# Performance work log

Measured on AMD Instinct MI355X. Metric: run time of the kernel, lower is better.

Reference implementation:

```python
import jax, jax.numpy as jnp
import numpy as np

B = 128
D_MODEL = 1024
D_HEAD = 1024


def setup_inputs() -> dict:
    key = jax.random.key(0)
    ks = jax.random.split(key, 12)
    w = 0.02  # weight init scale
    return {
        "x_t": jax.random.normal(ks[0], (B, D_MODEL), dtype=jnp.float32),
        "C_prev": jax.random.normal(ks[1], (B, D_HEAD, D_HEAD), dtype=jnp.float32) * 0.05,
        "n_prev": jax.random.normal(ks[2], (B, D_HEAD), dtype=jnp.float32) * 0.05,
        "m_prev": jax.random.normal(ks[3], (B,), dtype=jnp.float32),
        "W_q": jax.random.normal(ks[4], (D_HEAD, D_MODEL), dtype=jnp.float32) * w,
        "W_k": jax.random.normal(ks[5], (D_HEAD, D_MODEL), dtype=jnp.float32) * w,
        "W_v": jax.random.normal(ks[6], (D_HEAD, D_MODEL), dtype=jnp.float32) * w,
        "w_i_w": jax.random.normal(ks[7], (D_MODEL,), dtype=jnp.float32) * w,
        "w_i_b": jnp.zeros((), dtype=jnp.float32),
        "w_f_w": jax.random.normal(ks[8], (D_MODEL,), dtype=jnp.float32) * w,
        "w_f_b": jnp.zeros((), dtype=jnp.float32),
        "W_o_w": jax.random.normal(ks[9], (D_HEAD, D_MODEL), dtype=jnp.float32) * w,
        "W_o_b": jnp.zeros((D_HEAD,), dtype=jnp.float32),
        "out_proj_w": jax.random.normal(ks[10], (D_MODEL, D_HEAD), dtype=jnp.float32) * w,
    }


def reference(x_t, C_prev, n_prev, m_prev, W_q, W_k, W_v,
              w_i_w, w_i_b, w_f_w, w_f_b, W_o_w, W_o_b, out_proj_w):
    d_head = W_q.shape[0]
    scale = 1.0 / jnp.sqrt(jnp.asarray(d_head, dtype=x_t.dtype))

    # projections (nn.Linear: y = x @ W.T)
    q_t = (x_t @ W_q.T) * scale            # (B, d)
    k_t = (x_t @ W_k.T) * scale            # (B, d)
    v_t = x_t @ W_v.T                      # (B, d)
    z_i = x_t @ w_i_w + w_i_b              # (B,)
    z_f = x_t @ w_f_w + w_f_b              # (B,)

    # stabilized exp gating
    m_t = jnp.maximum(z_f + m_prev, z_i)   # (B,)
    i_p = jnp.exp(z_i - m_t)               # (B,)
    f_p = jnp.exp(z_f + m_prev - m_t)      # (B,)

    # rank-1 outer-product write to matrix memory
    outer = v_t[:, :, None] * k_t[:, None, :]                 # (B, d, d)
    C_t = f_p[:, None, None] * C_prev + i_p[:, None, None] * outer
    n_t = f_p[:, None] * n_prev + i_p[:, None] * k_t

    # matvec read + normalization
    o_t = jax.nn.sigmoid(x_t @ W_o_w.T + W_o_b)               # (B, d)
    Cq = jnp.einsum('bij,bj->bi', C_t, q_t)                   # (B, d)
    denom = jnp.maximum(jnp.abs(jnp.sum(n_t * q_t, axis=-1, keepdims=True)), 1.0)
    h_head = o_t * Cq / denom
    h_t = h_head @ out_proj_w.T                               # (B, d_model)
    return (h_t, C_t, n_t, m_t)
```

## Files before the change

### kernel.cpp

```cpp
#include <hip/hip_runtime.h>
#include <hip/hip_bf16.h>
#include <math.h>

#define B_SZ   128
#define D_DIM  1024

typedef float f32x4 __attribute__((ext_vector_type(4)));

#define WS_Q   0
#define WS_K   (131072)
#define WS_V   (262144)
#define WS_O   (393216)
#define WS_H   (524288)
#define WS_IP  (655360)
#define WS_FP  (655488)
#define WS_DEN (655616)

#define OUT_H  0
#define OUT_C  (131072)
#define OUT_N  (134348800)
#define OUT_M  (134479872)

__global__ __launch_bounds__(256) void gemm_proj(
    const float* __restrict__ x,
    const float* __restrict__ Wq, const float* __restrict__ Wk,
    const float* __restrict__ Wv, const float* __restrict__ Wo,
    const float* __restrict__ Wob,
    float* __restrict__ oq, float* __restrict__ okk,
    float* __restrict__ ov, float* __restrict__ oo)
{
    __shared__ float Xs[32][64];
    __shared__ float Ws[32][32];

    const int tid = threadIdx.x;
    const int m0 = blockIdx.y * 64;
    const int ng = blockIdx.x * 32;
    const int matsel = ng >> 10;
    const int n0 = ng & 1023;
    const float* __restrict__ W =
        (matsel == 0) ? Wq : (matsel == 1) ? Wk : (matsel == 2) ? Wv : Wo;

    const int tx = tid & 7;
    const int ty = tid >> 3;

    float acc[2][4] = {{0.f,0.f,0.f,0.f},{0.f,0.f,0.f,0.f}};

    for (int kp = 0; kp < 1024; kp += 32) {
        #pragma unroll
        for (int l = 0; l < 2; ++l) {
            int f = tid + l * 256;
            int row = f >> 3, c = f & 7;
            float4 v4 = *(const float4*)&x[(m0 + row) * 1024 + kp + 4 * c];
            Xs[4*c+0][row] = v4.x; Xs[4*c+1][row] = v4.y;
            Xs[4*c+2][row] = v4.z; Xs[4*c+3][row] = v4.w;
        }
        {
            int row = tid >> 3, c = tid & 7;
            float4 v4 = *(const float4*)&W[(n0 + row) * 1024 + kp + 4 * c];
            Ws[4*c+0][row] = v4.x; Ws[4*c+1][row] = v4.y;
            Ws[4*c+2][row] = v4.z; Ws[4*c+3][row] = v4.w;
        }
        __syncthreads();
        #pragma unroll
        for (int k = 0; k < 32; ++k) {
            float2 xv = *(const float2*)&Xs[k][2 * ty];
            float4 wv = *(const float4*)&Ws[k][4 * tx];
            acc[0][0] += xv.x * wv.x; acc[0][1] += xv.x * wv.y;
            acc[0][2] += xv.x * wv.z; acc[0][3] += xv.x * wv.w;
            acc[1][0] += xv.y * wv.x; acc[1][1] += xv.y * wv.y;
            acc[1][2] += xv.y * wv.z; acc[1][3] += xv.y * wv.w;
        }
        __syncthreads();
    }

    #pragma unroll
    for (int r = 0; r < 2; ++r) {
        int b = m0 + 2 * ty + r;
        #pragma unroll
        for (int i2 = 0; i2 < 4; ++i2) {
            int j = n0 + 4 * tx + i2;
            float v = acc[r][i2];
            if (matsel == 0)      oq[b * 1024 + j] = v * 0.03125f;
            else if (matsel == 1) okk[b * 1024 + j] = v * 0.03125f;
            else if (matsel == 2) ov[b * 1024 + j] = v;
            else { v += Wob[j]; oo[b * 1024 + j] = 1.0f / (1.0f + expf(-v)); }
        }
    }
}

__global__ __launch_bounds__(256) void gates_kernel(
    const float* __restrict__ x, const float* __restrict__ n_prev,
    const float* __restrict__ m_prev,
    const float* __restrict__ w_i, const float* __restrict__ b_i,
    const float* __restrict__ w_f, const float* __restrict__ b_f,
    const float* __restrict__ ws_k, const float* __restrict__ ws_q,
    float* __restrict__ out_n, float* __restrict__ out_m,
    float* __restrict__ ws_ip, float* __restrict__ ws_fp,
    float* __restrict__ ws_den)
{
    const int b = blockIdx.x;
    const int t = threadIdx.x;
    const int lane = t & 63, wave = t >> 6;

    __shared__ float red[8];
    __shared__ float bc[2];

    float4 xv = ((const float4*)(x + b * 1024))[t];
    float4 wi = ((const float4*)w_i)[t];
    float4 wf = ((const float4*)w_f)[t];
    float si = xv.x*wi.x + xv.y*wi.y + xv.z*wi.z + xv.w*wi.w;
    float sf = xv.x*wf.x + xv.y*wf.y + xv.z*wf.z + xv.w*wf.w;
    #pragma unroll
    for (int off = 32; off >= 1; off >>= 1) {
        si += __shfl_down(si, off);
        sf += __shfl_down(sf, off);
    }
    if (lane == 0) { red[wave] = si; red[4 + wave] = sf; }
    __syncthreads();
    if (t == 0) {
        float zi = red[0] + red[1] + red[2] + red[3] + b_i[0];
        float zf = red[4] + red[5] + red[6] + red[7] + b_f[0];
        float mp = m_prev[b];
        float mt = fmaxf(zf + mp, zi);
        float ip = expf(zi - mt);
        float fp = expf(zf + mp - mt);
        out_m[b] = mt; ws_ip[b] = ip; ws_fp[b] = fp;
        bc[0] = ip; bc[1] = fp;
    }
    __syncthreads();
    float ip = bc[0], fp = bc[1];
    float4 np = ((const float4*)(n_prev + b * 1024))[t];
    float4 kk = ((const float4*)(ws_k + b * 1024))[t];
    float4 qq = ((const float4*)(ws_q + b * 1024))[t];
    float4 nt;
    nt.x = fp * np.x + ip * kk.x;
    nt.y = fp * np.y + ip * kk.y;
    nt.z = fp * np.z + ip * kk.z;
    nt.w = fp * np.w + ip * kk.w;
    ((float4*)(out_n + b * 1024))[t] = nt;
    float sd = nt.x*qq.x + nt.y*qq.y + nt.z*qq.z + nt.w*qq.w;
    #pragma unroll
    for (int off = 32; off >= 1; off >>= 1) sd += __shfl_down(sd, off);
    if (lane == 0) red[wave] = sd;
    __syncthreads();
    if (t == 0) {
        float d = red[0] + red[1] + red[2] + red[3];
        ws_den[b] = fmaxf(fabsf(d), 1.0f);
    }
}

__global__ __launch_bounds__(256) void cell_kernel(
    const float* __restrict__ C_prev,
    const float* __restrict__ ws_k, const float* __restrict__ ws_q,
    const float* __restrict__ ws_v, const float* __restrict__ ws_o,
    const float* __restrict__ ws_ip, const float* __restrict__ ws_fp,
    const float* __restrict__ ws_den,
    float* __restrict__ out_C, float* __restrict__ ws_h)
{
    const int t    = threadIdx.x;
    const int lane = t & 63;
    const int wave = t >> 6;
    const int wglob = blockIdx.x * 4 + wave;
    const int r0 = wglob * 16;
    const int b  = r0 >> 10;

    const float fp   = ws_fp[b];
    const float ip   = ws_ip[b];
    const float rden = 1.0f / ws_den[b];

    const f32x4* qv = (const f32x4*)(ws_q + b * 1024);
    const f32x4* kv = (const f32x4*)(ws_k + b * 1024);
    f32x4 q4[4], k4[4];
    #pragma unroll
    for (int j = 0; j < 4; ++j) {
        q4[j] = qv[lane + 64 * j];
        k4[j] = kv[lane + 64 * j];
    }

    const f32x4* Cp = (const f32x4*)(C_prev + (size_t)r0 * 1024);
    f32x4*       Ct = (f32x4*)(out_C + (size_t)r0 * 1024);

    #define CELL_ROW(RR, CBUF)                                                \
    {                                                                         \
        const int row = r0 + (RR);                                            \
        const float coef = ip * ws_v[row];                                    \
        float s = 0.f;                                                        \
        _Pragma("unroll")                                                     \
        for (int j = 0; j < 4; ++j) {                                         \
            f32x4 r = fp * CBUF[j] + coef * k4[j];                            \
            __builtin_nontemporal_store(r, &Ct[(RR) * 256 + lane + 64 * j]);  \
            f32x4 d = r * q4[j];                                              \
            s += d.x + d.y + d.z + d.w;                                       \
        }                                                                     \
        _Pragma("unroll")                                                     \
        for (int off = 32; off >= 1; off >>= 1)                               \
            s += __shfl_xor(s, off);                                          \
        if (lane == 0)                                                        \
            ws_h[row] = ws_o[row] * s * rden;                                 \
    }

    f32x4 cA[4], cB[4];
    #pragma unroll
    for (int j = 0; j < 4; ++j)
        cA[j] = __builtin_nontemporal_load(&Cp[lane + 64 * j]);

    #pragma unroll
    for (int rr = 0; rr < 16; rr += 2) {
        #pragma unroll
        for (int j = 0; j < 4; ++j)
            cB[j] = __builtin_nontemporal_load(&Cp[(rr + 1) * 256 + lane + 64 * j]);
        CELL_ROW(rr, cA);
        if (rr + 2 < 16) {
            #pragma unroll
            for (int j = 0; j < 4; ++j)
                cA[j] = __builtin_nontemporal_load(&Cp[(rr + 2) * 256 + lane + 64 * j]);
        }
        CELL_ROW(rr + 1, cB);
    }
    #undef CELL_ROW
}

__global__ __launch_bounds__(256) void gemm_out(
    const float* __restrict__ A,
    const float* __restrict__ W,
    float* __restrict__ out)
{
    __shared__ float Xs[32][64];
    __shared__ float Ws[32][32];

    const int tid = threadIdx.x;
    const int m0 = blockIdx.y * 64;
    const int n0 = blockIdx.x * 32;
    const int tx = tid & 7;
    const int ty = tid >> 3;

    float acc[2][4] = {{0.f,0.f,0.f,0.f},{0.f,0.f,0.f,0.f}};

    for (int kp = 0; kp < 1024; kp += 32) {
        #pragma unroll
        for (int l = 0; l < 2; ++l) {
            int f = tid + l * 256;
            int row = f >> 3, c = f & 7;
            float4 v4 = *(const float4*)&A[(m0 + row) * 1024 + kp + 4 * c];
            Xs[4*c+0][row] = v4.x; Xs[4*c+1][row] = v4.y;
            Xs[4*c+2][row] = v4.z; Xs[4*c+3][row] = v4.w;
        }
        {
            int row = tid >> 3, c = tid & 7;
            float4 v4 = *(const float4*)&W[(n0 + row) * 1024 + kp + 4 * c];
            Ws[4*c+0][row] = v4.x; Ws[4*c+1][row] = v4.y;
            Ws[4*c+2][row] = v4.z; Ws[4*c+3][row] = v4.w;
        }
        __syncthreads();
        #pragma unroll
        for (int k = 0; k < 32; ++k) {
            float2 xv = *(const float2*)&Xs[k][2 * ty];
            float4 wv = *(const float4*)&Ws[k][4 * tx];
            acc[0][0] += xv.x * wv.x; acc[0][1] += xv.x * wv.y;
            acc[0][2] += xv.x * wv.z; acc[0][3] += xv.x * wv.w;
            acc[1][0] += xv.y * wv.x; acc[1][1] += xv.y * wv.y;
            acc[1][2] += xv.y * wv.z; acc[1][3] += xv.y * wv.w;
        }
        __syncthreads();
    }

    #pragma unroll
    for (int r = 0; r < 2; ++r) {
        int bb = m0 + 2 * ty + r;
        #pragma unroll
        for (int i2 = 0; i2 < 4; ++i2) {
            int j = n0 + 4 * tx + i2;
            out[bb * 1024 + j] = acc[r][i2];
        }
    }
}

extern "C" void kernel_launch(void* const* d_in, const int* in_sizes, int n_in,
                              void* d_out, int out_size, void* d_ws, size_t ws_size,
                              hipStream_t stream) {
    const float* x_t      = (const float*)d_in[0];
    const float* C_prev   = (const float*)d_in[1];
    const float* n_prev   = (const float*)d_in[2];
    const float* m_prev   = (const float*)d_in[3];
    const float* W_q      = (const float*)d_in[4];
    const float* W_k      = (const float*)d_in[5];
    const float* W_v      = (const float*)d_in[6];
    const float* w_i_w    = (const float*)d_in[7];
    const float* w_i_b    = (const float*)d_in[8];
    const float* w_f_w    = (const float*)d_in[9];
    const float* w_f_b    = (const float*)d_in[10];
    const float* W_o_w    = (const float*)d_in[11];
    const float* W_o_b    = (const float*)d_in[12];
    const float* out_proj = (const float*)d_in[13];

    float* out = (float*)d_out;
    float* ws  = (float*)d_ws;

    float* ws_q   = ws + WS_Q;
    float* ws_k   = ws + WS_K;
    float* ws_v   = ws + WS_V;
    float* ws_o   = ws + WS_O;
    float* ws_h   = ws + WS_H;
    float* ws_ip  = ws + WS_IP;
    float* ws_fp  = ws + WS_FP;
    float* ws_den = ws + WS_DEN;

    gemm_proj<<<dim3(128, 2), 256, 0, stream>>>(
        x_t, W_q, W_k, W_v, W_o_w, W_o_b, ws_q, ws_k, ws_v, ws_o);

    gates_kernel<<<128, 256, 0, stream>>>(
        x_t, n_prev, m_prev, w_i_w, w_i_b, w_f_w, w_f_b,
        ws_k, ws_q, out + OUT_N, out + OUT_M, ws_ip, ws_fp, ws_den);

    cell_kernel<<<2048, 256, 0, stream>>>(
        C_prev, ws_k, ws_q, ws_v, ws_o, ws_ip, ws_fp, ws_den,
        out + OUT_C, ws_h);

    gemm_out<<<dim3(32, 2), 256, 0, stream>>>(ws_h, out_proj, out + OUT_H);
}
```

Measured before the change: 976.7 us.

## Fuse gates into cell kernel, prefetch GEMM tiles, retile output GEMM

The gates/normalizer computation now runs inside the cell kernel. Each of the 16 blocks per batch row recomputes the gate values and the denominator redundantly, and one elected block writes n and m. This removes a kernel launch and the workspace round-trip, at the cost of redundant small reductions per block. Both GEMMs now prefetch the next k-tile into registers before computing on the current one. The output GEMM uses 32-row tiles so it launches twice as many blocks.

```diff
diff --git a/kernel.cpp b/kernel.cpp
--- a/kernel.cpp
+++ b/kernel.cpp
@@ -12,9 +12,6 @@
 #define WS_V   (262144)
 #define WS_O   (393216)
 #define WS_H   (524288)
-#define WS_IP  (655360)
-#define WS_FP  (655488)
-#define WS_DEN (655616)
 
 #define OUT_H  0
 #define OUT_C  (131072)
@@ -43,24 +40,31 @@
     const int tx = tid & 7;
     const int ty = tid >> 3;
 
+    const int xrow0 = tid >> 3,          xc0 = tid & 7;
+    const int xrow1 = (tid + 256) >> 3,  xc1 = tid & 7;
+    const int wrow  = tid >> 3,          wc  = tid & 7;
+
     float acc[2][4] = {{0.f,0.f,0.f,0.f},{0.f,0.f,0.f,0.f}};
 
+    float4 xr0 = *(const float4*)&x[(m0 + xrow0) * 1024 + 4 * xc0];
+    float4 xr1 = *(const float4*)&x[(m0 + xrow1) * 1024 + 4 * xc1];
+    float4 wr  = *(const float4*)&W[(n0 + wrow) * 1024 + 4 * wc];
+
     for (int kp = 0; kp < 1024; kp += 32) {
-        #pragma unroll
-        for (int l = 0; l < 2; ++l) {
-            int f = tid + l * 256;
-            int row = f >> 3, c = f & 7;
-            float4 v4 = *(const float4*)&x[(m0 + row) * 1024 + kp + 4 * c];
-            Xs[4*c+0][row] = v4.x; Xs[4*c+1][row] = v4.y;
-            Xs[4*c+2][row] = v4.z; Xs[4*c+3][row] = v4.w;
-        }
-        {
-            int row = tid >> 3, c = tid & 7;
-            float4 v4 = *(const float4*)&W[(n0 + row) * 1024 + kp + 4 * c];
-            Ws[4*c+0][row] = v4.x; Ws[4*c+1][row] = v4.y;
-            Ws[4*c+2][row] = v4.z; Ws[4*c+3][row] = v4.w;
-        }
-        __syncthreads();
+        Xs[4*xc0+0][xrow0] = xr0.x; Xs[4*xc0+1][xrow0] = xr0.y;
+        Xs[4*xc0+2][xrow0] = xr0.z; Xs[4*xc0+3][xrow0] = xr0.w;
+        Xs[4*xc1+0][xrow1] = xr1.x; Xs[4*xc1+1][xrow1] = xr1.y;
+        Xs[4*xc1+2][xrow1] = xr1.z; Xs[4*xc1+3][xrow1] = xr1.w;
+        Ws[4*wc+0][wrow] = wr.x; Ws[4*wc+1][wrow] = wr.y;
+        Ws[4*wc+2][wrow] = wr.z; Ws[4*wc+3][wrow] = wr.w;
+        __syncthreads();
+
+        if (kp + 32 < 1024) {
+            xr0 = *(const float4*)&x[(m0 + xrow0) * 1024 + kp + 32 + 4 * xc0];
+            xr1 = *(const float4*)&x[(m0 + xrow1) * 1024 + kp + 32 + 4 * xc1];
+            wr  = *(const float4*)&W[(n0 + wrow) * 1024 + kp + 32 + 4 * wc];
+        }
+
         #pragma unroll
         for (int k = 0; k < 32; ++k) {
             float2 xv = *(const float2*)&Xs[k][2 * ty];
@@ -88,85 +92,78 @@
     }
 }
 
-__global__ __launch_bounds__(256) void gates_kernel(
+__global__ __launch_bounds__(256) void cell_kernel(
     const float* __restrict__ x, const float* __restrict__ n_prev,
     const float* __restrict__ m_prev,
     const float* __restrict__ w_i, const float* __restrict__ b_i,
     const float* __restrict__ w_f, const float* __restrict__ b_f,
-    const float* __restrict__ ws_k, const float* __restrict__ ws_q,
-    float* __restrict__ out_n, float* __restrict__ out_m,
-    float* __restrict__ ws_ip, float* __restrict__ ws_fp,
-    float* __restrict__ ws_den)
-{
-    const int b = blockIdx.x;
-    const int t = threadIdx.x;
-    const int lane = t & 63, wave = t >> 6;
-
-    __shared__ float red[8];
-    __shared__ float bc[2];
-
-    float4 xv = ((const float4*)(x + b * 1024))[t];
-    float4 wi = ((const float4*)w_i)[t];
-    float4 wf = ((const float4*)w_f)[t];
-    float si = xv.x*wi.x + xv.y*wi.y + xv.z*wi.z + xv.w*wi.w;
-    float sf = xv.x*wf.x + xv.y*wf.y + xv.z*wf.z + xv.w*wf.w;
-    #pragma unroll
-    for (int off = 32; off >= 1; off >>= 1) {
-        si += __shfl_down(si, off);
-        sf += __shfl_down(sf, off);
-    }
-    if (lane == 0) { red[wave] = si; red[4 + wave] = sf; }
-    __syncthreads();
-    if (t == 0) {
-        float zi = red[0] + red[1] + red[2] + red[3] + b_i[0];
-        float zf = red[4] + red[5] + red[6] + red[7] + b_f[0];
-        float mp = m_prev[b];
-        float mt = fmaxf(zf + mp, zi);
-        float ip = expf(zi - mt);
-        float fp = expf(zf + mp - mt);
-        out_m[b] = mt; ws_ip[b] = ip; ws_fp[b] = fp;
-        bc[0] = ip; bc[1] = fp;
-    }
-    __syncthreads();
-    float ip = bc[0], fp = bc[1];
-    float4 np = ((const float4*)(n_prev + b * 1024))[t];
-    float4 kk = ((const float4*)(ws_k + b * 1024))[t];
-    float4 qq = ((const float4*)(ws_q + b * 1024))[t];
-    float4 nt;
-    nt.x = fp * np.x + ip * kk.x;
-    nt.y = fp * np.y + ip * kk.y;
-    nt.z = fp * np.z + ip * kk.z;
-    nt.w = fp * np.w + ip * kk.w;
-    ((float4*)(out_n + b * 1024))[t] = nt;
-    float sd = nt.x*qq.x + nt.y*qq.y + nt.z*qq.z + nt.w*qq.w;
-    #pragma unroll
-    for (int off = 32; off >= 1; off >>= 1) sd += __shfl_down(sd, off);
-    if (lane == 0) red[wave] = sd;
-    __syncthreads();
-    if (t == 0) {
-        float d = red[0] + red[1] + red[2] + red[3];
-        ws_den[b] = fmaxf(fabsf(d), 1.0f);
-    }
-}
-
-__global__ __launch_bounds__(256) void cell_kernel(
     const float* __restrict__ C_prev,
     const float* __restrict__ ws_k, const float* __restrict__ ws_q,
     const float* __restrict__ ws_v, const float* __restrict__ ws_o,
-    const float* __restrict__ ws_ip, const float* __restrict__ ws_fp,
-    const float* __restrict__ ws_den,
-    float* __restrict__ out_C, float* __restrict__ ws_h)
+    float* __restrict__ out_C, float* __restrict__ out_n,
+    float* __restrict__ out_m, float* __restrict__ ws_h)
 {
     const int t    = threadIdx.x;
     const int lane = t & 63;
     const int wave = t >> 6;
+    const int b    = blockIdx.x >> 4;
+    const bool elected = (blockIdx.x & 15) == 0;
+
+    __shared__ float red[8];
+    __shared__ float bc[4];
+
+    {
+        float4 xv = ((const float4*)(x + b * 1024))[t];
+        float4 wi = ((const float4*)w_i)[t];
+        float4 wf = ((const float4*)w_f)[t];
+        float si = xv.x*wi.x + xv.y*wi.y + xv.z*wi.z + xv.w*wi.w;
+        float sf = xv.x*wf.x + xv.y*wf.y + xv.z*wf.z + xv.w*wf.w;
+        #pragma unroll
+        for (int off = 32; off >= 1; off >>= 1) {
+            si += __shfl_down(si, off);
+            sf += __shfl_down(sf, off);
+        }
+        if (lane == 0) { red[wave] = si; red[4 + wave] = sf; }
+        __syncthreads();
+        if (t == 0) {
+            float zi = red[0] + red[1] + red[2] + red[3] + b_i[0];
+            float zf = red[4] + red[5] + red[6] + red[7] + b_f[0];
+            float mp = m_prev[b];
+            float mt = fmaxf(zf + mp, zi);
+            float ipv = expf(zi - mt);
+            float fpv = expf(zf + mp - mt);
+            bc[0] = ipv; bc[1] = fpv;
+            if (elected) out_m[b] = mt;
+        }
+        __syncthreads();
+        float ipv = bc[0], fpv = bc[1];
+        float4 np = ((const float4*)(n_prev + b * 1024))[t];
+        float4 kk = ((const float4*)(ws_k + b * 1024))[t];
+        float4 qq = ((const float4*)(ws_q + b * 1024))[t];
+        float4 nt;
+        nt.x = fpv * np.x + ipv * kk.x;
+        nt.y = fpv * np.y + ipv * kk.y;
+        nt.z = fpv * np.z + ipv * kk.z;
+        nt.w = fpv * np.w + ipv * kk.w;
+        if (elected) ((float4*)(out_n + b * 1024))[t] = nt;
+        float sd = nt.x*qq.x + nt.y*qq.y + nt.z*qq.z + nt.w*qq.w;
+        #pragma unroll
+        for (int off = 32; off >= 1; off >>= 1) sd += __shfl_down(sd, off);
+        if (lane == 0) red[wave] = sd;
+        __syncthreads();
+        if (t == 0) {
+            float d = red[0] + red[1] + red[2] + red[3];
+            bc[2] = 1.0f / fmaxf(fabsf(d), 1.0f);
+        }
+        __syncthreads();
+    }
+
+    const float ip   = bc[0];
+    const float fp   = bc[1];
+    const float rden = bc[2];
+
     const int wglob = blockIdx.x * 4 + wave;
     const int r0 = wglob * 16;
-    const int b  = r0 >> 10;
-
-    const float fp   = ws_fp[b];
-    const float ip   = ws_ip[b];
-    const float rden = 1.0f / ws_den[b];
 
     const f32x4* qv = (const f32x4*)(ws_q + b * 1024);
     const f32x4* kv = (const f32x4*)(ws_k + b * 1024);
@@ -225,54 +222,49 @@
     const float* __restrict__ W,
     float* __restrict__ out)
 {
-    __shared__ float Xs[32][64];
+    __shared__ float Xs[32][32];
     __shared__ float Ws[32][32];
 
     const int tid = threadIdx.x;
-    const int m0 = blockIdx.y * 64;
+    const int m0 = blockIdx.y * 32;
     const int n0 = blockIdx.x * 32;
     const int tx = tid & 7;
     const int ty = tid >> 3;
 
-    float acc[2][4] = {{0.f,0.f,0.f,0.f},{0.f,0.f,0.f,0.f}};
+    const int xrow = tid >> 3, xc = tid & 7;
+    const int wrow = tid >> 3, wc = tid & 7;
+
+    float acc[4] = {0.f, 0.f, 0.f, 0.f};
+
+    float4 xr = *(const float4*)&A[(m0 + xrow) * 1024 + 4 * xc];
+    float4 wr = *(const float4*)&W[(n0 + wrow) * 1024 + 4 * wc];
 
     for (int kp = 0; kp < 1024; kp += 32) {
-        #pragma unroll
-        for (int l = 0; l < 2; ++l) {
-            int f = tid + l * 256;
-            int row = f >> 3, c = f & 7;
-            float4 v4 = *(const float4*)&A[(m0 + row) * 1024 + kp + 4 * c];
-            Xs[4*c+0][row] = v4.x; Xs[4*c+1][row] = v4.y;
-            Xs[4*c+2][row] = v4.z; Xs[4*c+3][row] = v4.w;
-        }
-        {
-            int row = tid >> 3, c = tid & 7;
-            float4 v4 = *(const float4*)&W[(n0 + row) * 1024 + kp + 4 * c];
-            Ws[4*c+0][row] = v4.x; Ws[4*c+1][row] = v4.y;
-            Ws[4*c+2][row] = v4.z; Ws[4*c+3][row] = v4.w;
-        }
-        __syncthreads();
+        Xs[4*xc+0][xrow] = xr.x; Xs[4*xc+1][xrow] = xr.y;
+        Xs[4*xc+2][xrow] = xr.z; Xs[4*xc+3][xrow] = xr.w;
+        Ws[4*wc+0][wrow] = wr.x; Ws[4*wc+1][wrow] = wr.y;
+        Ws[4*wc+2][wrow] = wr.z; Ws[4*wc+3][wrow] = wr.w;
+        __syncthreads();
+
+        if (kp + 32 < 1024) {
+            xr = *(const float4*)&A[(m0 + xrow) * 1024 + kp + 32 + 4 * xc];
+            wr = *(const float4*)&W[(n0 + wrow) * 1024 + kp + 32 + 4 * wc];
+        }
+
         #pragma unroll
         for (int k = 0; k < 32; ++k) {
-            float2 xv = *(const float2*)&Xs[k][2 * ty];
+            float  xv = Xs[k][ty];
             float4 wv = *(const float4*)&Ws[k][4 * tx];
-            acc[0][0] += xv.x * wv.x; acc[0][1] += xv.x * wv.y;
-            acc[0][2] += xv.x * wv.z; acc[0][3] += xv.x * wv.w;
-            acc[1][0] += xv.y * wv.x; acc[1][1] += xv.y * wv.y;
-            acc[1][2] += xv.y * wv.z; acc[1][3] += xv.y * wv.w;
-        }
-        __syncthreads();
-    }
-
-    #pragma unroll
-    for (int r = 0; r < 2; ++r) {
-        int bb = m0 + 2 * ty + r;
-        #pragma unroll
-        for (int i2 = 0; i2 < 4; ++i2) {
-            int j = n0 + 4 * tx + i2;
-            out[bb * 1024 + j] = acc[r][i2];
-        }
-    }
+            acc[0] += xv * wv.x; acc[1] += xv * wv.y;
+            acc[2] += xv * wv.z; acc[3] += xv * wv.w;
+        }
+        __syncthreads();
+    }
+
+    const int bb = m0 + ty;
+    #pragma unroll
+    for (int i2 = 0; i2 < 4; ++i2)
+        out[bb * 1024 + n0 + 4 * tx + i2] = acc[i2];
 }
 
 extern "C" void kernel_launch(void* const* d_in, const int* in_sizes, int n_in,
@@ -296,25 +288,19 @@
     float* out = (float*)d_out;
     float* ws  = (float*)d_ws;
 
-    float* ws_q   = ws + WS_Q;
-    float* ws_k   = ws + WS_K;
-    float* ws_v   = ws + WS_V;
-    float* ws_o   = ws + WS_O;
-    float* ws_h   = ws + WS_H;
-    float* ws_ip  = ws + WS_IP;
-    float* ws_fp  = ws + WS_FP;
-    float* ws_den = ws + WS_DEN;
+    float* ws_q = ws + WS_Q;
+    float* ws_k = ws + WS_K;
+    float* ws_v = ws + WS_V;
+    float* ws_o = ws + WS_O;
+    float* ws_h = ws + WS_H;
 
     gemm_proj<<<dim3(128, 2), 256, 0, stream>>>(
         x_t, W_q, W_k, W_v, W_o_w, W_o_b, ws_q, ws_k, ws_v, ws_o);
 
-    gates_kernel<<<128, 256, 0, stream>>>(
+    cell_kernel<<<2048, 256, 0, stream>>>(
         x_t, n_prev, m_prev, w_i_w, w_i_b, w_f_w, w_f_b,
-        ws_k, ws_q, out + OUT_N, out + OUT_M, ws_ip, ws_fp, ws_den);
-
-    cell_kernel<<<2048, 256, 0, stream>>>(
-        C_prev, ws_k, ws_q, ws_v, ws_o, ws_ip, ws_fp, ws_den,
-        out + OUT_C, ws_h);
-
-    gemm_out<<<dim3(32, 2), 256, 0, stream>>>(ws_h, out_proj, out + OUT_H);
+        C_prev, ws_k, ws_q, ws_v, ws_o,
+        out + OUT_C, out + OUT_N, out + OUT_M, ws_h);
+
+    gemm_out<<<dim3(32, 4), 256, 0, stream>>>(ws_h, out_proj, out + OUT_H);
 }
```

After: 951.6 us. 1.03x faster.
